# Optimization experiments

Measured on AMD Instinct MI355X. Metric: run time of the kernel, lower is better.

Reference implementation:

```python
import jax, jax.numpy as jnp
import numpy as np

N_NODES = 50000
N_EDGES = 800000
IN_FEATS = 128
N_HIDDEN = 128
N_CLASSES = 16


def setup_inputs() -> dict:
    key = jax.random.key(0)
    ks = jax.random.split(key, 10)
    d = {
        'x': jax.random.normal(ks[0], (N_NODES, IN_FEATS), dtype=jnp.float32),
        'src': jax.random.randint(ks[1], (N_EDGES,), 0, N_NODES, dtype=jnp.int32),
        'dst': jax.random.randint(ks[2], (N_EDGES,), 0, N_NODES, dtype=jnp.int32),
    }
    sc = 1.0 / np.sqrt(N_HIDDEN)
    d['w_self0'] = jax.random.normal(ks[3], (IN_FEATS, N_HIDDEN), dtype=jnp.float32) * sc
    d['w_neigh0'] = jax.random.normal(ks[4], (IN_FEATS, N_HIDDEN), dtype=jnp.float32) * sc
    d['b0'] = jnp.zeros((N_HIDDEN,), dtype=jnp.float32)
    d['w_self1'] = jax.random.normal(ks[5], (N_HIDDEN, N_HIDDEN), dtype=jnp.float32) * sc
    d['w_neigh1'] = jax.random.normal(ks[6], (N_HIDDEN, N_HIDDEN), dtype=jnp.float32) * sc
    d['b1'] = jnp.zeros((N_HIDDEN,), dtype=jnp.float32)
    d['w_self2'] = jax.random.normal(ks[7], (N_HIDDEN, N_HIDDEN), dtype=jnp.float32) * sc
    d['w_neigh2'] = jax.random.normal(ks[8], (N_HIDDEN, N_HIDDEN), dtype=jnp.float32) * sc
    d['b2'] = jnp.zeros((N_HIDDEN,), dtype=jnp.float32)
    d['w_head'] = jax.random.normal(ks[9], (N_HIDDEN, N_CLASSES), dtype=jnp.float32) * sc
    d['b_head'] = jnp.zeros((N_CLASSES,), dtype=jnp.float32)
    return d


def _sage_conv(h, src, dst, inv_deg, w_self, w_neigh, b):
    # mean aggregator: gather src features, scatter-add to dst, divide by in-degree
    agg = jax.ops.segment_sum(h[src], dst, num_segments=N_NODES)  # [N, d]
    neigh = agg * inv_deg[:, None]
    return h @ w_self + neigh @ w_neigh + b


def reference(x, src, dst, w_self0, w_neigh0, b0, w_self1, w_neigh1, b1,
              w_self2, w_neigh2, b2, w_head, b_head):
    deg = jax.ops.segment_sum(jnp.ones((src.shape[0],), jnp.float32), dst,
                              num_segments=N_NODES)
    inv_deg = 1.0 / jnp.maximum(deg, 1.0)
    h = x  # dropout is identity in eval mode
    for (ws, wn, b) in ((w_self0, w_neigh0, b0),
                        (w_self1, w_neigh1, b1),
                        (w_self2, w_neigh2, b2)):
        h = jax.nn.relu(_sage_conv(h, src, dst, inv_deg, ws, wn, b))
    pls = jnp.mean(h, axis=0, keepdims=True)  # AvgPooling over single graph -> [1, n_hidden]
    score = pls @ w_head + b_head  # [1, n_classes]
    return (score, pls)
```

## Files before the change

kernel.cpp:

```cpp
#include <hip/hip_runtime.h>
#include <hip/hip_bf16.h>
#include <hip/hip_fp8.h>
#include <stdint.h>

#define NN 50000
#define NE 800000
#define F 128
#define NCLS 16
#define NB 196
#define BCAP 5120
#define PA_EPT 16

typedef __attribute__((ext_vector_type(8))) short short8;
typedef __attribute__((ext_vector_type(4))) float f32x4;
typedef __attribute__((ext_vector_type(2))) float f32x2;
typedef __attribute__((ext_vector_type(4))) unsigned int uint4v;

#define OB_COLSUM    0u
#define OB_BCUR      512u
#define OB_BBASE     1536u
#define OB_ROWSTART  4096u
#define OB_INVDEG    204800u
#define OB_PAIRS     409600u
#define OB_SRCS16    4423680u
#define OB_WT        6023680u
#define OB_XB        6220800u
#define OB_HB1       19020800u
#define OB_X8        31820800u
#define OB_F8A       38220800u
#define OB_NB        44620800u

__device__ __forceinline__ uint32_t swz_off(uint32_t row, uint32_t k) {
    uint32_t c = ((k >> 5) << 2) | ((k >> 2) & 3u);
    uint32_t b = (((k >> 4) & 1u) << 3) | ((k & 3u) << 1);
    return (row << 8) + (((c ^ (row & 15u)) << 4) | b);
}

__device__ __forceinline__ uint32_t pack_bf2(float a, float b) {
    __hip_bfloat16 l = __float2bfloat16(a), h = __float2bfloat16(b);
    return ((uint32_t)(*(uint16_t*)&h) << 16) | (uint32_t)(*(uint16_t*)&l);
}

__device__ __forceinline__ uint8_t f32_to_fp8(float v) {
#if __has_builtin(__builtin_amdgcn_cvt_pk_fp8_f32)
    return (uint8_t)(__builtin_amdgcn_cvt_pk_fp8_f32(v, 0.f, 0, false) & 0xff);
#else
    __hip_fp8_e4m3 t(v);
    return t.__x;
#endif
}

__device__ __forceinline__ uint32_t f32x4_to_fp8x4(float a, float b, float c, float d) {
#if __has_builtin(__builtin_amdgcn_cvt_pk_fp8_f32)
    int r = __builtin_amdgcn_cvt_pk_fp8_f32(a, b, 0, false);
    r = __builtin_amdgcn_cvt_pk_fp8_f32(c, d, r, true);
    return (uint32_t)r;
#else
    __hip_fp8_e4m3 ta(a), tb(b), tc(c), td(d);
    return (uint32_t)ta.__x | ((uint32_t)tb.__x << 8) | ((uint32_t)tc.__x << 16) | ((uint32_t)td.__x << 24);
#endif
}

__device__ __forceinline__ void fp8x4_to_f32(uint32_t d, float& f0, float& f1, float& f2, float& f3) {
#if __has_builtin(__builtin_amdgcn_cvt_pk_f32_fp8)
    f32x2 lo = __builtin_amdgcn_cvt_pk_f32_fp8((int)d, false);
    f32x2 hi = __builtin_amdgcn_cvt_pk_f32_fp8((int)d, true);
    f0 = lo.x; f1 = lo.y; f2 = hi.x; f3 = hi.y;
#else
    __hip_fp8_e4m3 t0, t1, t2, t3;
    t0.__x = (uint8_t)(d & 0xff); t1.__x = (uint8_t)((d >> 8) & 0xff);
    t2.__x = (uint8_t)((d >> 16) & 0xff); t3.__x = (uint8_t)((d >> 24) & 0xff);
    f0 = (float)t0; f1 = (float)t1; f2 = (float)t2; f3 = (float)t3;
#endif
}

__global__ void init_kernel(float* __restrict__ colsum, int* __restrict__ bcur) {
    int t = threadIdx.x;
    if (t < 128) colsum[t] = 0.f;
    if (t < NB) bcur[t] = t * BCAP;
}

__global__ __launch_bounds__(256) void convert_x2(const float* __restrict__ x,
                                                  uint8_t* __restrict__ xb,
                                                  uint8_t* __restrict__ x8) {
    int t = blockIdx.x * 256 + threadIdx.x;
    uint32_t row = (uint32_t)t >> 5;
    uint32_t q = (uint32_t)t & 31u;
    float4 v = *(const float4*)(x + row * F + q * 4);
    uint32_t c = ((q >> 3) << 2) | (q & 3u);
    uint32_t hi = (q >> 2) & 1u;
    uint2 pk;
    pk.x = pack_bf2(v.x, v.y);
    pk.y = pack_bf2(v.z, v.w);
    *(uint2*)(xb + (row << 8) + (((c ^ (row & 15u)) << 4) | (hi << 3))) = pk;
    *(uint32_t*)(x8 + row * 128u + q * 4u) = f32x4_to_fp8x4(v.x, v.y, v.z, v.w);
}

__global__ __launch_bounds__(256) void prep_w(const float* __restrict__ w0, const float* __restrict__ w1,
                                              const float* __restrict__ w2, const float* __restrict__ w3,
                                              const float* __restrict__ w4, const float* __restrict__ w5,
                                              uint8_t* __restrict__ wt) {
    int m = blockIdx.y;
    const float* w = m == 0 ? w0 : m == 1 ? w1 : m == 2 ? w2 : m == 3 ? w3 : m == 4 ? w4 : w5;
    int t = blockIdx.x * 256 + threadIdx.x;
    int n = t >> 6;
    int k0 = (t & 63) << 1;
    uint32_t pk = pack_bf2(w[k0 * F + n], w[(k0 + 1) * F + n]);
    *(uint32_t*)(wt + (uint32_t)m * 32768u + swz_off((uint32_t)n, (uint32_t)k0)) = pk;
}

__global__ __launch_bounds__(256) void pass_a(const int* __restrict__ src,
                                              const int* __restrict__ dst,
                                              int* __restrict__ bcur,
                                              uint32_t* __restrict__ pairs) {
    __shared__ int cnt[NB];
    __shared__ int base_s[NB];
    int t = threadIdx.x;
    for (int i = t; i < NB; i += 256) cnt[i] = 0;
    __syncthreads();

    uint32_t pk[PA_EPT];
    int bk[PA_EPT];
    int e0 = blockIdx.x * (256 * PA_EPT) + t;
#pragma unroll
    for (int j = 0; j < PA_EPT; ++j) {
        int e = e0 + j * 256;
        if (e < NE) {
            int sv = src[e], dv = dst[e];
            bk[j] = dv >> 8;
            pk[j] = (uint32_t)sv | (((uint32_t)dv & 255u) << 16);
            atomicAdd(&cnt[bk[j]], 1);
        } else bk[j] = -1;
    }
    __syncthreads();
    for (int i = t; i < NB; i += 256) {
        if (cnt[i] > 0) base_s[i] = atomicAdd(&bcur[i], cnt[i]);
        cnt[i] = 0;
    }
    __syncthreads();
#pragma unroll
    for (int j = 0; j < PA_EPT; ++j) {
        if (bk[j] >= 0) {
            int pos = base_s[bk[j]] + atomicAdd(&cnt[bk[j]], 1);
            pairs[pos] = pk[j];
        }
    }
}

__global__ __launch_bounds__(256) void bucket_scan(const int* __restrict__ bcur,
                                                   int* __restrict__ bbase,
                                                   int* __restrict__ row_start) {
    __shared__ int s[256];
    int t = threadIdx.x;
    int fill = (t < NB) ? (bcur[t] - t * BCAP) : 0;
    s[t] = fill;
    __syncthreads();
    for (int off = 1; off < 256; off <<= 1) {
        int u = (t >= off) ? s[t - off] : 0;
        __syncthreads();
        s[t] += u;
        __syncthreads();
    }
    if (t < NB) bbase[t] = s[t] - fill;
    if (t == 0) row_start[NN] = NE;
}

__global__ __launch_bounds__(256) void pass_b(const uint32_t* __restrict__ pairs,
                                              const int* __restrict__ bcur,
                                              const int* __restrict__ bbase,
                                              int* __restrict__ row_start,
                                              float* __restrict__ inv_deg,
                                              unsigned short* __restrict__ srcs) {
    __shared__ int cnt[256];
    __shared__ int s[256];
    __shared__ int cur[256];
    int b = blockIdx.x, t = threadIdx.x;
    int in0 = b * BCAP;
    int fill = bcur[b] - in0;
    int out0 = bbase[b];
    cnt[t] = 0;
    __syncthreads();
    for (int i = t; i < fill; i += 256)
        atomicAdd(&cnt[pairs[in0 + i] >> 16], 1);
    __syncthreads();
    int v = cnt[t];
    s[t] = v;
    __syncthreads();
    for (int off = 1; off < 256; off <<= 1) {
        int u = (t >= off) ? s[t - off] : 0;
        __syncthreads();
        s[t] += u;
        __syncthreads();
    }
    int excl = s[t] - v;
    cur[t] = out0 + excl;
    int row = (b << 8) + t;
    if (row < NN) {
        row_start[row] = out0 + excl;
        inv_deg[row] = 1.0f / (float)(v > 1 ? v : 1);
    }
    __syncthreads();
    for (int i = t; i < fill; i += 256) {
        uint32_t p = pairs[in0 + i];
        int pos = atomicAdd(&cur[p >> 16], 1);
        srcs[pos] = (unsigned short)(p & 0xffffu);
    }
}

__global__ __launch_bounds__(256) void aggregate_f8(
        const uint8_t* __restrict__ hf8, const int* __restrict__ row_start,
        const unsigned short* __restrict__ srcs, const float* __restrict__ inv_deg,
        uint8_t* __restrict__ nb) {
    int node = blockIdx.x * 4 + (threadIdx.x >> 6);
    int l = threadIdx.x & 63;
    int half = l >> 5;
    uint32_t sub = (uint32_t)(l & 31);
    const uint8_t* base = hf8 + sub * 4u;
    int e0 = row_start[node], e1 = row_start[node + 1];
    float a0 = 0.f, a1 = 0.f, a2 = 0.f, a3 = 0.f;

    int e = e0 + half;
    for (; e + 6 < e1; e += 8) {
        uint32_t s0 = srcs[e], s1 = srcs[e + 2], s2 = srcs[e + 4], s3 = srcs[e + 6];
        uint32_t d0 = *(const uint32_t*)(base + ((uint32_t)s0 << 7));
        uint32_t d1 = *(const uint32_t*)(base + ((uint32_t)s1 << 7));
        uint32_t d2 = *(const uint32_t*)(base + ((uint32_t)s2 << 7));
        uint32_t d3 = *(const uint32_t*)(base + ((uint32_t)s3 << 7));
        float f0, f1, f2, f3;
        fp8x4_to_f32(d0, f0, f1, f2, f3); a0 += f0; a1 += f1; a2 += f2; a3 += f3;
        fp8x4_to_f32(d1, f0, f1, f2, f3); a0 += f0; a1 += f1; a2 += f2; a3 += f3;
        fp8x4_to_f32(d2, f0, f1, f2, f3); a0 += f0; a1 += f1; a2 += f2; a3 += f3;
        fp8x4_to_f32(d3, f0, f1, f2, f3); a0 += f0; a1 += f1; a2 += f2; a3 += f3;
    }
    for (; e < e1; e += 2) {
        uint32_t s0 = srcs[e];
        uint32_t d0 = *(const uint32_t*)(base + ((uint32_t)s0 << 7));
        float f0, f1, f2, f3;
        fp8x4_to_f32(d0, f0, f1, f2, f3); a0 += f0; a1 += f1; a2 += f2; a3 += f3;
    }
    a0 += __shfl_xor(a0, 32);
    a1 += __shfl_xor(a1, 32);
    a2 += __shfl_xor(a2, 32);
    a3 += __shfl_xor(a3, 32);
    if (half == 0) {
        float idg = inv_deg[node];
        uint32_t c = ((sub >> 3) << 2) | (sub & 3u);
        uint32_t hi8 = ((sub >> 2) & 1u) << 3;
        uint2 pk;
        pk.x = pack_bf2(a0 * idg, a1 * idg);
        pk.y = pack_bf2(a2 * idg, a3 * idg);
        *(uint2*)(nb + ((uint32_t)node << 8) +
                  (((c ^ ((uint32_t)node & 15u)) << 4) | hi8)) = pk;
    }
}

__global__ __launch_bounds__(256) void gemm_mfma(
        const uint8_t* __restrict__ a_self, const uint8_t* __restrict__ a_neigh,
        const uint8_t* __restrict__ wt_self, const uint8_t* __restrict__ wt_neigh,
        const float* __restrict__ bias, uint8_t* __restrict__ hout,
        uint8_t* hout_f8, float* colsum) {
    __shared__ uint4v As4[1024];
    __shared__ uint4v Ws4[2048];
    __shared__ float cs[128];
    int tid = threadIdx.x;
    int lane = tid & 63, wave = tid >> 6;
    int rl = lane & 15, g = lane >> 4;
    int row0 = blockIdx.x * 64;

    f32x4 acc[8];
    f32x4 z = {0.f, 0.f, 0.f, 0.f};
#pragma unroll
    for (int nt = 0; nt < 8; ++nt) acc[nt] = z;

    const char* AsB = (const char*)As4;
    const char* WsB = (const char*)Ws4;

#pragma unroll
    for (int pass = 0; pass < 2; ++pass) {
        if (pass) __syncthreads();
        const uint4v* ga = (const uint4v*)((pass ? a_neigh : a_self) + (size_t)row0 * 256);
        const uint4v* gw = (const uint4v*)(pass ? wt_neigh : wt_self);
#pragma unroll
        for (int i = 0; i < 4; ++i) As4[tid + i * 256] = ga[tid + i * 256];
#pragma unroll
        for (int i = 0; i < 8; ++i) Ws4[tid + i * 256] = gw[tid + i * 256];
        __syncthreads();
#pragma unroll
        for (int ks = 0; ks < 4; ++ks) {
            int chunk = ((ks << 2) | g) ^ rl;
            short8 a = *(const short8*)(AsB + ((wave * 16 + rl) << 8) + (chunk << 4));
#pragma unroll
            for (int nt = 0; nt < 8; ++nt) {
                short8 bb = *(const short8*)(WsB + ((nt * 16 + rl) << 8) + (chunk << 4));
                acc[nt] = __builtin_amdgcn_mfma_f32_16x16x32_bf16(a, bb, acc[nt], 0, 0, 0);
            }
        }
    }

    bool doCol = (colsum != nullptr);
    bool doF8 = (hout_f8 != nullptr);
    if (doCol) {
        if (tid < 128) cs[tid] = 0.f;
        __syncthreads();
    }
#pragma unroll
    for (int nt = 0; nt < 8; ++nt) {
        int col = nt * 16 + rl;
        float bv = bias[col];
        float rsum = 0.f;
#pragma unroll
        for (int i = 0; i < 4; ++i) {
            int row = row0 + wave * 16 + g * 4 + i;
            if (row < NN) {
                float v = fmaxf(acc[nt][i] + bv, 0.f);
                rsum += v;
                *(__hip_bfloat16*)(hout + swz_off((uint32_t)row, (uint32_t)col)) =
                    __float2bfloat16(v);
                if (doF8) hout_f8[(uint32_t)row * 128u + (uint32_t)col] = f32_to_fp8(v);
            }
        }
        if (doCol) atomicAdd(&cs[col], rsum);
    }
    if (doCol) {
        __syncthreads();
        if (tid < 128) atomicAdd(&colsum[tid], cs[tid]);
    }
}

__global__ __launch_bounds__(128) void head_kernel(const float* __restrict__ colsum,
                                                   const float* __restrict__ w_head,
                                                   const float* __restrict__ b_head,
                                                   float* __restrict__ out) {
    __shared__ float pls[F];
    int t = threadIdx.x;
    float p = colsum[t] * (1.0f / (float)NN);
    pls[t] = p;
    out[NCLS + t] = p;
    __syncthreads();
    if (t < NCLS) {
        float sc = b_head[t];
        for (int f = 0; f < F; ++f) sc += pls[f] * w_head[f * NCLS + t];
        out[t] = sc;
    }
}

extern "C" void kernel_launch(void* const* d_in, const int* in_sizes, int n_in,
                              void* d_out, int out_size, void* d_ws, size_t ws_size,
                              hipStream_t stream) {
    const float* x       = (const float*)d_in[0];
    const int*   src     = (const int*)d_in[1];
    const int*   dst     = (const int*)d_in[2];
    const float* w_self0 = (const float*)d_in[3];
    const float* w_neigh0= (const float*)d_in[4];
    const float* b0      = (const float*)d_in[5];
    const float* w_self1 = (const float*)d_in[6];
    const float* w_neigh1= (const float*)d_in[7];
    const float* b1      = (const float*)d_in[8];
    const float* w_self2 = (const float*)d_in[9];
    const float* w_neigh2= (const float*)d_in[10];
    const float* b2      = (const float*)d_in[11];
    const float* w_head  = (const float*)d_in[12];
    const float* b_head  = (const float*)d_in[13];
    float* out = (float*)d_out;

    uint8_t* ws = (uint8_t*)d_ws;
    float* colsum   = (float*)(ws + OB_COLSUM);
    int*   bcur     = (int*)(ws + OB_BCUR);
    int*   bbase    = (int*)(ws + OB_BBASE);
    int*   row_start= (int*)(ws + OB_ROWSTART);
    float* inv_deg  = (float*)(ws + OB_INVDEG);
    uint32_t* pairs = (uint32_t*)(ws + OB_PAIRS);
    unsigned short* srcs16 = (unsigned short*)(ws + OB_SRCS16);
    uint8_t* wt     = ws + OB_WT;
    uint8_t* xb     = ws + OB_XB;
    uint8_t* hb1    = ws + OB_HB1;
    uint8_t* x8     = ws + OB_X8;
    uint8_t* f8a    = ws + OB_F8A;
    uint8_t* nb     = ws + OB_NB;

    init_kernel<<<1, 256, 0, stream>>>(colsum, bcur);
    convert_x2<<<6250, 256, 0, stream>>>(x, xb, x8);
    prep_w<<<dim3(32, 6), 256, 0, stream>>>(w_self0, w_neigh0, w_self1, w_neigh1,
                                            w_self2, w_neigh2, wt);
    pass_a<<<NB, 256, 0, stream>>>(src, dst, bcur, pairs);
    bucket_scan<<<1, 256, 0, stream>>>(bcur, bbase, row_start);
    pass_b<<<NB, 256, 0, stream>>>(pairs, bcur, bbase, row_start, inv_deg, srcs16);

    const int GB = (NN + 63) / 64;

    aggregate_f8<<<12500, 256, 0, stream>>>(x8, row_start, srcs16, inv_deg, nb);
    gemm_mfma<<<GB, 256, 0, stream>>>(xb, nb, wt + 0 * 32768, wt + 1 * 32768, b0,
                                      hb1, f8a, nullptr);
    aggregate_f8<<<12500, 256, 0, stream>>>(f8a, row_start, srcs16, inv_deg, nb);
    gemm_mfma<<<GB, 256, 0, stream>>>(hb1, nb, wt + 2 * 32768, wt + 3 * 32768, b1,
                                      xb, x8, nullptr);
    aggregate_f8<<<12500, 256, 0, stream>>>(x8, row_start, srcs16, inv_deg, nb);
    gemm_mfma<<<GB, 256, 0, stream>>>(xb, nb, wt + 4 * 32768, wt + 5 * 32768, b2,
                                      hb1, nullptr, colsum);

    head_kernel<<<1, 128, 0, stream>>>(colsum, w_head, b_head, out);
}
```

Measured before the change: 208.6 us.

## Fold init into convert, widen aggregate gathers, use direct global-to-LDS loads

Merges the init kernel into convert_x2's first block, which removes one launch. The fp8 aggregation now gives each lane 8 bytes (16 lanes per row, 4 edge groups) instead of 4 bytes across two halves. That halves the number of gather instructions per edge but adds one more shuffle reduction stage. The GEMM tile loads now use global_load_lds so data goes from global memory straight into LDS without passing through registers. The direct LDS load is issued without any explicit wait on its completion before the barrier, which may be a correctness risk depending on what the compiler inserts.

```diff
diff --git a/kernel.cpp b/kernel.cpp
--- a/kernel.cpp
+++ b/kernel.cpp
@@ -74,15 +74,22 @@
 #endif
 }
 
-__global__ void init_kernel(float* __restrict__ colsum, int* __restrict__ bcur) {
-    int t = threadIdx.x;
-    if (t < 128) colsum[t] = 0.f;
-    if (t < NB) bcur[t] = t * BCAP;
+__device__ __forceinline__ void gload16(const void* g, void* l) {
+    __builtin_amdgcn_global_load_lds(
+        (const __attribute__((address_space(1))) unsigned int*)g,
+        (__attribute__((address_space(3))) unsigned int*)l, 16, 0, 0);
 }
 
 __global__ __launch_bounds__(256) void convert_x2(const float* __restrict__ x,
                                                   uint8_t* __restrict__ xb,
-                                                  uint8_t* __restrict__ x8) {
+                                                  uint8_t* __restrict__ x8,
+                                                  float* __restrict__ colsum,
+                                                  int* __restrict__ bcur) {
+    if (blockIdx.x == 0) {
+        int tt = threadIdx.x;
+        if (tt < 128) colsum[tt] = 0.f;
+        if (tt < NB) bcur[tt] = tt * BCAP;
+    }
     int t = blockIdx.x * 256 + threadIdx.x;
     uint32_t row = (uint32_t)t >> 5;
     uint32_t q = (uint32_t)t & 31u;
@@ -213,44 +220,55 @@
         uint8_t* __restrict__ nb) {
     int node = blockIdx.x * 4 + (threadIdx.x >> 6);
     int l = threadIdx.x & 63;
-    int half = l >> 5;
-    uint32_t sub = (uint32_t)(l & 31);
-    const uint8_t* base = hf8 + sub * 4u;
+    int g = l >> 4;
+    uint32_t m = (uint32_t)(l & 15);
+    const uint8_t* base = hf8 + m * 8u;
     int e0 = row_start[node], e1 = row_start[node + 1];
-    float a0 = 0.f, a1 = 0.f, a2 = 0.f, a3 = 0.f;
-
-    int e = e0 + half;
-    for (; e + 6 < e1; e += 8) {
-        uint32_t s0 = srcs[e], s1 = srcs[e + 2], s2 = srcs[e + 4], s3 = srcs[e + 6];
-        uint32_t d0 = *(const uint32_t*)(base + ((uint32_t)s0 << 7));
-        uint32_t d1 = *(const uint32_t*)(base + ((uint32_t)s1 << 7));
-        uint32_t d2 = *(const uint32_t*)(base + ((uint32_t)s2 << 7));
-        uint32_t d3 = *(const uint32_t*)(base + ((uint32_t)s3 << 7));
+    float a0=0.f,a1=0.f,a2=0.f,a3=0.f,a4=0.f,a5=0.f,a6=0.f,a7=0.f;
+
+    int e = e0 + g;
+    for (; e + 4 < e1; e += 8) {
+        uint32_t sa = srcs[e];
+        uint32_t sb = srcs[e + 4];
+        uint2 da = *(const uint2*)(base + ((uint32_t)sa << 7));
+        uint2 db = *(const uint2*)(base + ((uint32_t)sb << 7));
         float f0, f1, f2, f3;
-        fp8x4_to_f32(d0, f0, f1, f2, f3); a0 += f0; a1 += f1; a2 += f2; a3 += f3;
-        fp8x4_to_f32(d1, f0, f1, f2, f3); a0 += f0; a1 += f1; a2 += f2; a3 += f3;
-        fp8x4_to_f32(d2, f0, f1, f2, f3); a0 += f0; a1 += f1; a2 += f2; a3 += f3;
-        fp8x4_to_f32(d3, f0, f1, f2, f3); a0 += f0; a1 += f1; a2 += f2; a3 += f3;
-    }
-    for (; e < e1; e += 2) {
-        uint32_t s0 = srcs[e];
-        uint32_t d0 = *(const uint32_t*)(base + ((uint32_t)s0 << 7));
+        fp8x4_to_f32(da.x, f0,f1,f2,f3); a0+=f0; a1+=f1; a2+=f2; a3+=f3;
+        fp8x4_to_f32(da.y, f0,f1,f2,f3); a4+=f0; a5+=f1; a6+=f2; a7+=f3;
+        fp8x4_to_f32(db.x, f0,f1,f2,f3); a0+=f0; a1+=f1; a2+=f2; a3+=f3;
+        fp8x4_to_f32(db.y, f0,f1,f2,f3); a4+=f0; a5+=f1; a6+=f2; a7+=f3;
+    }
+    if (e < e1) {
+        uint32_t sa = srcs[e];
+        uint2 da = *(const uint2*)(base + ((uint32_t)sa << 7));
         float f0, f1, f2, f3;
-        fp8x4_to_f32(d0, f0, f1, f2, f3); a0 += f0; a1 += f1; a2 += f2; a3 += f3;
-    }
-    a0 += __shfl_xor(a0, 32);
-    a1 += __shfl_xor(a1, 32);
-    a2 += __shfl_xor(a2, 32);
-    a3 += __shfl_xor(a3, 32);
-    if (half == 0) {
+        fp8x4_to_f32(da.x, f0,f1,f2,f3); a0+=f0; a1+=f1; a2+=f2; a3+=f3;
+        fp8x4_to_f32(da.y, f0,f1,f2,f3); a4+=f0; a5+=f1; a6+=f2; a7+=f3;
+    }
+    a0 += __shfl_xor(a0, 16); a1 += __shfl_xor(a1, 16);
+    a2 += __shfl_xor(a2, 16); a3 += __shfl_xor(a3, 16);
+    a4 += __shfl_xor(a4, 16); a5 += __shfl_xor(a5, 16);
+    a6 += __shfl_xor(a6, 16); a7 += __shfl_xor(a7, 16);
+    a0 += __shfl_xor(a0, 32); a1 += __shfl_xor(a1, 32);
+    a2 += __shfl_xor(a2, 32); a3 += __shfl_xor(a3, 32);
+    a4 += __shfl_xor(a4, 32); a5 += __shfl_xor(a5, 32);
+    a6 += __shfl_xor(a6, 32); a7 += __shfl_xor(a7, 32);
+
+    if (g == 0) {
         float idg = inv_deg[node];
-        uint32_t c = ((sub >> 3) << 2) | (sub & 3u);
-        uint32_t hi8 = ((sub >> 2) & 1u) << 3;
-        uint2 pk;
-        pk.x = pack_bf2(a0 * idg, a1 * idg);
-        pk.y = pack_bf2(a2 * idg, a3 * idg);
-        *(uint2*)(nb + ((uint32_t)node << 8) +
-                  (((c ^ ((uint32_t)node & 15u)) << 4) | hi8)) = pk;
+        uint2 w0, w1;
+        w0.x = pack_bf2(a0 * idg, a1 * idg);
+        w0.y = pack_bf2(a2 * idg, a3 * idg);
+        w1.x = pack_bf2(a4 * idg, a5 * idg);
+        w1.y = pack_bf2(a6 * idg, a7 * idg);
+        uint32_t c1 = m >> 2;
+        uint32_t h  = (m >> 1) & 1u;
+        uint32_t ca = (c1 << 2) | ((2u * m) & 3u);
+        uint32_t cb = (c1 << 2) | ((2u * m + 1u) & 3u);
+        uint32_t rx = (uint32_t)node & 15u;
+        char* rowp = (char*)nb + ((uint32_t)node << 8);
+        *(uint2*)(rowp + (((ca ^ rx) << 4) | (h << 3))) = w0;
+        *(uint2*)(rowp + (((cb ^ rx) << 4) | (h << 3))) = w1;
     }
 }
 
@@ -281,9 +299,9 @@
         const uint4v* ga = (const uint4v*)((pass ? a_neigh : a_self) + (size_t)row0 * 256);
         const uint4v* gw = (const uint4v*)(pass ? wt_neigh : wt_self);
 #pragma unroll
-        for (int i = 0; i < 4; ++i) As4[tid + i * 256] = ga[tid + i * 256];
-#pragma unroll
-        for (int i = 0; i < 8; ++i) Ws4[tid + i * 256] = gw[tid + i * 256];
+        for (int i = 0; i < 4; ++i) gload16(&ga[tid + i * 256], &As4[tid + i * 256]);
+#pragma unroll
+        for (int i = 0; i < 8; ++i) gload16(&gw[tid + i * 256], &Ws4[tid + i * 256]);
         __syncthreads();
 #pragma unroll
         for (int ks = 0; ks < 4; ++ks) {
@@ -378,8 +396,7 @@
     uint8_t* f8a    = ws + OB_F8A;
     uint8_t* nb     = ws + OB_NB;
 
-    init_kernel<<<1, 256, 0, stream>>>(colsum, bcur);
-    convert_x2<<<6250, 256, 0, stream>>>(x, xb, x8);
+    convert_x2<<<6250, 256, 0, stream>>>(x, xb, x8, colsum, bcur);
     prep_w<<<dim3(32, 6), 256, 0, stream>>>(w_self0, w_neigh0, w_self1, w_neigh1,
                                             w_self2, w_neigh2, wt);
     pass_a<<<NB, 256, 0, stream>>>(src, dst, bcur, pairs);
```

After: 198.9 us. -4.6%, faster.
